# Kernel tuning notes

Measured on AMD Instinct MI355X. Metric: run time of the kernel, lower is better.

## Reference

```python
import jax, jax.numpy as jnp
import numpy as np

N_EMBD = 1024
N_HEAD = 16
HEAD_DIM = N_EMBD // N_HEAD


def setup_inputs() -> dict:
    key = jax.random.key(0)
    ks = jax.random.split(key, 9)
    B, T, C = 4, 2048, N_EMBD
    s = 1.0 / np.sqrt(C)
    return {
        "x": jax.random.normal(ks[0], (B, T, C), jnp.float32),
        "Wq": jax.random.normal(ks[1], (C, C), jnp.float32) * s,
        "bq": jnp.zeros((C,), jnp.float32),
        "Wk": jax.random.normal(ks[2], (C, C), jnp.float32) * s,
        "bk": jnp.zeros((C,), jnp.float32),
        "Wv": jax.random.normal(ks[3], (C, C), jnp.float32) * s,
        "bv": jnp.zeros((C,), jnp.float32),
        "Wp": jax.random.normal(ks[4], (C, C), jnp.float32) * s,
        "bp": jnp.zeros((C,), jnp.float32),
    }


def reference(x, Wq, bq, Wk, bk, Wv, bv, Wp, bp):
    B, T, C = x.shape
    H, D = N_HEAD, HEAD_DIM
    # QKV projections -> (B, H, T, D)
    q = (x @ Wq + bq).reshape(B, T, H, D).transpose(0, 2, 1, 3)
    k = (x @ Wk + bk).reshape(B, T, H, D).transpose(0, 2, 1, 3)
    v = (x @ Wv + bv).reshape(B, T, H, D).transpose(0, 2, 1, 3)
    # scaled scores with causal mask
    att = jnp.einsum("bhtd,bhsd->bhts", q, k) / jnp.sqrt(jnp.asarray(D, x.dtype))
    causal = jnp.tril(jnp.ones((T, T), bool))
    att = jnp.where(causal, att, jnp.asarray(-jnp.inf, att.dtype))
    att = jax.nn.softmax(att, axis=-1)
    # dropout is identity in eval/reference mode
    out = jnp.einsum("bhts,bhsd->bhtd", att, v)
    out = out.transpose(0, 2, 1, 3).reshape(B, T, C)
    return out @ Wp + bp
```

## Files before the change

### kernel.cpp

```cpp
#include <hip/hip_runtime.h>
#include <stdint.h>


typedef __attribute__((ext_vector_type(8))) short bf16x8;
typedef __attribute__((ext_vector_type(8))) ushort u16x8;
typedef __attribute__((ext_vector_type(4))) float f32x4;

__device__ __forceinline__ ushort f2bf(float f) {
  union { float f; uint32_t i; } c; c.f = f;
  uint32_t r = c.i + 0x7fffu + ((c.i >> 16) & 1u);
  return (ushort)(r >> 16);
}
__device__ __forceinline__ uint32_t cvt_pk_bf16(float lo, float hi) {
  uint32_t r;
  asm("v_cvt_pk_bf16_f32 %0, %1, %2" : "=v"(r) : "v"(lo), "v"(hi));
  return r;
}

#define GLOAD16(gp, lp)                                                          \
  __builtin_amdgcn_global_load_lds(                                              \
      (const __attribute__((address_space(1))) unsigned int*)(gp),               \
      (__attribute__((address_space(3))) unsigned int*)(lp), 16, 0, 0)

__global__ __launch_bounds__(256) void f32_to_bf16(const float* __restrict__ in,
                                                   ushort* __restrict__ out, int n) {
  const int i = (blockIdx.x * 256 + threadIdx.x) * 8;
  if (i + 8 > n) return;
  float4 a = *(const float4*)(in + i);
  float4 b = *(const float4*)(in + i + 4);
  u16x8 r;
  r[0] = f2bf(a.x); r[1] = f2bf(a.y); r[2] = f2bf(a.z); r[3] = f2bf(a.w);
  r[4] = f2bf(b.x); r[5] = f2bf(b.y); r[6] = f2bf(b.z); r[7] = f2bf(b.w);
  *(u16x8*)(out + i) = r;
}

__global__ __launch_bounds__(256) void transpose_f32_bf16(const float* __restrict__ W,
                                                          ushort* __restrict__ Wt) {
  __shared__ ushort tile[32][33];
  const int k0 = blockIdx.x * 32, n0 = blockIdx.y * 32;
  const int tx = threadIdx.x & 31, ty = threadIdx.x >> 5;
#pragma unroll
  for (int i = 0; i < 4; ++i)
    tile[ty + i * 8][tx] = f2bf(W[(size_t)(k0 + ty + i * 8) * 1024 + n0 + tx]);
  __syncthreads();
#pragma unroll
  for (int i = 0; i < 4; ++i)
    Wt[(size_t)(n0 + ty + i * 8) * 1024 + k0 + tx] = tile[tx][ty + i * 8];
}

template <int MODE>
__global__ __launch_bounds__(256) void gemm_bt(const ushort* __restrict__ A,
                                               const ushort* __restrict__ Bt,
                                               const float* __restrict__ bias,
                                               void* __restrict__ outp,
                                               int M, int N, int K) {
  __shared__ ushort As[128][32];
  __shared__ ushort Bs[128][32];
  const int tid = threadIdx.x;
  const int lane = tid & 63, wave = tid >> 6;
  const int quad = lane >> 4, l16 = lane & 15;
  const int wy = wave >> 1, wx = wave & 1;
  const int m0 = blockIdx.y * 128, n0 = blockIdx.x * 128;

  const f32x4 fzero = {0.f, 0.f, 0.f, 0.f};
  f32x4 acc[4][4];
#pragma unroll
  for (int i = 0; i < 4; ++i)
#pragma unroll
    for (int j = 0; j < 4; ++j) acc[i][j] = fzero;

  const int r = lane >> 2, ch = (lane & 3) * 8;
  const ushort* Abase = A + (size_t)(m0 + wave * 32 + r) * K + ch;
  const ushort* Bbase = Bt + (size_t)(n0 + wave * 32 + r) * K + ch;

  const int nk = K >> 5;
  for (int kt = 0; kt < nk; ++kt) {
    __syncthreads();
    GLOAD16(Abase + kt * 32,          &As[wave * 32][0]);
    GLOAD16(Abase + 16 * K + kt * 32, &As[wave * 32 + 16][0]);
    GLOAD16(Bbase + kt * 32,          &Bs[wave * 32][0]);
    GLOAD16(Bbase + 16 * K + kt * 32, &Bs[wave * 32 + 16][0]);
    __syncthreads();

    bf16x8 af[4], bfr[4];
#pragma unroll
    for (int i = 0; i < 4; ++i)
      af[i] = *(const bf16x8*)&As[wy * 64 + i * 16 + l16][quad * 8];
#pragma unroll
    for (int j = 0; j < 4; ++j)
      bfr[j] = *(const bf16x8*)&Bs[wx * 64 + j * 16 + l16][quad * 8];
#pragma unroll
    for (int i = 0; i < 4; ++i)
#pragma unroll
      for (int j = 0; j < 4; ++j)
        acc[i][j] = __builtin_amdgcn_mfma_f32_16x16x32_bf16(af[i], bfr[j], acc[i][j], 0, 0, 0);
  }

#pragma unroll
  for (int j = 0; j < 4; ++j) {
    const int col = n0 + wx * 64 + j * 16 + l16;
    const float bv = bias[col];
#pragma unroll
    for (int i = 0; i < 4; ++i) {
#pragma unroll
      for (int rr = 0; rr < 4; ++rr) {
        const int row = m0 + wy * 64 + i * 16 + quad * 4 + rr;
        const float v = acc[i][j][rr] + bv;
        if (MODE == 0) {
          ((float*)outp)[(size_t)row * N + col] = v;
        } else {
          ushort* out = (ushort*)outp;
          const int b = row >> 11, t = row & 2047, h = col >> 6, d = col & 63;
          if (MODE == 1)
            out[(((size_t)(b * 16 + h) * 2048) + t) * 64 + d] = f2bf(v);
          else
            out[(((size_t)(b * 16 + h) * 64) + d) * 2048 + t] = f2bf(v);
        }
      }
    }
  }
}

__global__ __launch_bounds__(256, 3) void attn_kernel(const ushort* __restrict__ q,
                                                      const ushort* __restrict__ k,
                                                      const ushort* __restrict__ v,
                                                      ushort* __restrict__ y) {
  const int T = 2048;
  const int bh = blockIdx.y;
  const int tid = threadIdx.x;
  const int lane = tid & 63, wave = tid >> 6;
  const int quad = lane >> 4, l16 = lane & 15;
  const int rr = lane >> 3, c8 = lane & 7;
  const int swz = l16 & 7;

  __shared__ ushort Qs[128][64];
  __shared__ ushort Ks[64][64];
  __shared__ ushort Vs[64][64];

  const ushort* qp = q + (size_t)bh * T * 64;
  const ushort* kp = k + (size_t)bh * T * 64;
  const ushort* vp = v + (size_t)bh * 64 * T;
  const int b = bh >> 4, h = bh & 15;

  ushort* Pw = &Qs[wave * 32][0];

  const f32x4 fzero = {0.f, 0.f, 0.f, 0.f};
  const float SC = 0.125f * 1.4426950408889634f;

  for (int qsel = 0; qsel < 2; ++qsel) {
    const int qt = qsel ? (15 - (int)blockIdx.x) : (int)blockIdx.x;
    const int qbase = qt * 128;

    __syncthreads();
#pragma unroll
    for (int t = 0; t < 4; ++t) {
      const int row = wave * 32 + t * 8 + rr;
      const int gc = c8 ^ (row & 7);
      GLOAD16(qp + (size_t)(qbase + row) * 64 + gc * 8, &Qs[wave * 32 + t * 8][0]);
    }
    __syncthreads();

    bf16x8 aq[2][2];
#pragma unroll
    for (int i = 0; i < 2; ++i)
#pragma unroll
      for (int kk = 0; kk < 2; ++kk)
        aq[i][kk] = *(const bf16x8*)&Qs[wave * 32 + i * 16 + l16][((4 * kk + quad) ^ swz) * 8];

    f32x4 acc_o[2][4];
    float mstate[2], lstate[2];
#pragma unroll
    for (int i = 0; i < 2; ++i) {
      mstate[i] = -1e30f; lstate[i] = 0.f;
#pragma unroll
      for (int jd = 0; jd < 4; ++jd) acc_o[i][jd] = fzero;
    }

    const int trow0 = qbase + wave * 32;
    const int nkt = qt * 2 + 2;

    for (int kt = 0; kt < nkt; ++kt) {
      __syncthreads();
#pragma unroll
      for (int t = 0; t < 2; ++t) {
        const int row = wave * 16 + t * 8 + rr;
        const int gc = c8 ^ (row & 7);
        GLOAD16(kp + (size_t)(kt * 64 + row) * 64 + gc * 8, &Ks[wave * 16 + t * 8][0]);
        GLOAD16(vp + (size_t)row * T + kt * 64 + gc * 8,    &Vs[wave * 16 + t * 8][0]);
      }
      __syncthreads();

      if (kt * 64 > trow0 + 31) continue;

      bf16x8 ak[4][2];
#pragma unroll
      for (int j = 0; j < 4; ++j)
#pragma unroll
        for (int kk = 0; kk < 2; ++kk)
          ak[j][kk] = *(const bf16x8*)&Ks[j * 16 + l16][((4 * kk + quad) ^ swz) * 8];

#pragma unroll
      for (int i = 0; i < 2; ++i) {
        const int tmin = trow0 + i * 16;
        if (kt * 64 > tmin + 15) continue;
        const int tglob = tmin + l16;

        f32x4 st[4];
#pragma unroll
        for (int j = 0; j < 4; ++j) st[j] = fzero;
#pragma unroll
        for (int j = 0; j < 4; ++j)
#pragma unroll
          for (int kk = 0; kk < 2; ++kk)
            st[j] = __builtin_amdgcn_mfma_f32_16x16x32_bf16(ak[j][kk], aq[i][kk], st[j], 0, 0, 0);

        float mp = -1e30f;
        const bool needmask = (kt * 64 + 63 > tmin);
        if (needmask) {
#pragma unroll
          for (int j = 0; j < 4; ++j)
#pragma unroll
            for (int r2 = 0; r2 < 4; ++r2) {
              const int sg = kt * 64 + j * 16 + quad * 4 + r2;
              float xv = st[j][r2] * SC;
              if (sg > tglob) xv = -1e30f;
              st[j][r2] = xv;
              mp = fmaxf(mp, xv);
            }
        } else {
#pragma unroll
          for (int j = 0; j < 4; ++j)
#pragma unroll
            for (int r2 = 0; r2 < 4; ++r2) {
              const float xv = st[j][r2] * SC;
              st[j][r2] = xv;
              mp = fmaxf(mp, xv);
            }
        }
        mp = fmaxf(mp, __shfl_xor(mp, 16, 64));
        mp = fmaxf(mp, __shfl_xor(mp, 32, 64));

        float mloc = mstate[i];
        const bool defer = (__all(mp - mloc <= 8.0f) != 0);
        if (!defer) {
          const float mnew = fmaxf(mloc, mp);
          const float alpha = exp2f(mloc - mnew);
          mstate[i] = mnew;
          lstate[i] *= alpha;
#pragma unroll
          for (int jd = 0; jd < 4; ++jd) acc_o[i][jd] *= alpha;
          mloc = mnew;
        }
        float rs = 0.f;
#pragma unroll
        for (int j = 0; j < 4; ++j)
#pragma unroll
          for (int r2 = 0; r2 < 4; ++r2) {
            const float p = exp2f(st[j][r2] - mloc);
            st[j][r2] = p;
            rs += p;
          }
        rs += __shfl_xor(rs, 16, 64);
        rs += __shfl_xor(rs, 32, 64);
        lstate[i] += rs;

        ushort* prow = Pw + l16 * 64;
#pragma unroll
        for (int j = 0; j < 4; ++j) {
          uint2 w2;
          w2.x = cvt_pk_bf16(st[j][0], st[j][1]);
          w2.y = cvt_pk_bf16(st[j][2], st[j][3]);
          const int cb = 2 * j + (quad >> 1);
          *(uint2*)(prow + ((cb ^ swz) << 3) + ((quad & 1) << 2)) = w2;
        }
        bf16x8 pb0 = *(const bf16x8*)(prow + ((quad ^ swz) << 3));
        bf16x8 pb1 = *(const bf16x8*)(prow + (((4 + quad) ^ swz) << 3));

#pragma unroll
        for (int jd = 0; jd < 4; ++jd) {
          const int vrow = jd * 16 + l16;
          bf16x8 av0 = *(const bf16x8*)&Vs[vrow][((quad) ^ swz) * 8];
          bf16x8 av1 = *(const bf16x8*)&Vs[vrow][((4 + quad) ^ swz) * 8];
          acc_o[i][jd] = __builtin_amdgcn_mfma_f32_16x16x32_bf16(av0, pb0, acc_o[i][jd], 0, 0, 0);
          acc_o[i][jd] = __builtin_amdgcn_mfma_f32_16x16x32_bf16(av1, pb1, acc_o[i][jd], 0, 0, 0);
        }
      }
    }

#pragma unroll
    for (int i = 0; i < 2; ++i) {
      const int t = trow0 + i * 16 + l16;
      const float inv = 1.0f / lstate[i];
#pragma unroll
      for (int jd = 0; jd < 4; ++jd) {
        uint2 w;
        w.x = cvt_pk_bf16(acc_o[i][jd][0] * inv, acc_o[i][jd][1] * inv);
        w.y = cvt_pk_bf16(acc_o[i][jd][2] * inv, acc_o[i][jd][3] * inv);
        *(uint2*)&y[((size_t)(b * 2048 + t)) * 1024 + h * 64 + jd * 16 + quad * 4] = w;
      }
    }
  }
}

extern "C" void kernel_launch(void* const* d_in, const int* in_sizes, int n_in,
                              void* d_out, int out_size, void* d_ws, size_t ws_size,
                              hipStream_t stream) {
  const float* x  = (const float*)d_in[0];
  const float* Wq = (const float*)d_in[1];
  const float* bq = (const float*)d_in[2];
  const float* Wk = (const float*)d_in[3];
  const float* bk = (const float*)d_in[4];
  const float* Wv = (const float*)d_in[5];
  const float* bv = (const float*)d_in[6];
  const float* Wp = (const float*)d_in[7];
  const float* bp = (const float*)d_in[8];

  ushort* ws  = (ushort*)d_ws;
  ushort* wqt = ws;
  ushort* wkt = wqt + (size_t)1024 * 1024;
  ushort* wvt = wkt + (size_t)1024 * 1024;
  ushort* wpt = wvt + (size_t)1024 * 1024;
  ushort* xb  = wpt + (size_t)1024 * 1024;
  ushort* qq  = xb + (size_t)8192 * 1024;
  ushort* kk  = qq + (size_t)8192 * 1024;
  ushort* vv  = kk + (size_t)8192 * 1024;
  ushort* y   = vv + (size_t)8192 * 1024;

  const dim3 tb(256);
  hipLaunchKernelGGL(f32_to_bf16, dim3(4096), tb, 0, stream, x, xb, 8192 * 1024);
  const dim3 tg(32, 32);
  hipLaunchKernelGGL(transpose_f32_bf16, tg, tb, 0, stream, Wq, wqt);
  hipLaunchKernelGGL(transpose_f32_bf16, tg, tb, 0, stream, Wk, wkt);
  hipLaunchKernelGGL(transpose_f32_bf16, tg, tb, 0, stream, Wv, wvt);
  hipLaunchKernelGGL(transpose_f32_bf16, tg, tb, 0, stream, Wp, wpt);

  const dim3 gg(8, 64);
  hipLaunchKernelGGL((gemm_bt<1>), gg, tb, 0, stream, xb, wqt, bq, (void*)qq, 8192, 1024, 1024);
  hipLaunchKernelGGL((gemm_bt<1>), gg, tb, 0, stream, xb, wkt, bk, (void*)kk, 8192, 1024, 1024);
  hipLaunchKernelGGL((gemm_bt<2>), gg, tb, 0, stream, xb, wvt, bv, (void*)vv, 8192, 1024, 1024);

  const dim3 ag(8, 64);
  hipLaunchKernelGGL(attn_kernel, ag, tb, 0, stream, qq, kk, vv, y);

  hipLaunchKernelGGL((gemm_bt<0>), gg, tb, 0, stream, y, wpt, bp, d_out, 8192, 1024, 1024);
}
```

Baseline: 329.5 us.

## Double-buffer LDS tiles in GEMM and attention, swap grid dimension order

Both the GEMM and the attention kernel now keep two LDS buffers and prefetch the next K/V (or A/B) tile into one while computing on the other. This cuts the per-iteration barrier count from two to one and lets global-to-LDS loads overlap with MFMA work. The grid axes are also swapped so consecutive block IDs walk the M/batch-head dimension, which changes the block scheduling order and cache locality. The cost is double the LDS footprint, which may reduce occupancy in the attention kernel.

```diff
diff --git a/kernel.cpp b/kernel.cpp
--- a/kernel.cpp
+++ b/kernel.cpp
@@ -54,13 +54,13 @@
                                                const float* __restrict__ bias,
                                                void* __restrict__ outp,
                                                int M, int N, int K) {
-  __shared__ ushort As[128][32];
-  __shared__ ushort Bs[128][32];
+  __shared__ ushort As[2][128][32];
+  __shared__ ushort Bs[2][128][32];
   const int tid = threadIdx.x;
   const int lane = tid & 63, wave = tid >> 6;
   const int quad = lane >> 4, l16 = lane & 15;
   const int wy = wave >> 1, wx = wave & 1;
-  const int m0 = blockIdx.y * 128, n0 = blockIdx.x * 128;
+  const int m0 = blockIdx.x * 128, n0 = blockIdx.y * 128;
 
   const f32x4 fzero = {0.f, 0.f, 0.f, 0.f};
   f32x4 acc[4][4];
@@ -73,27 +73,37 @@
   const ushort* Abase = A + (size_t)(m0 + wave * 32 + r) * K + ch;
   const ushort* Bbase = Bt + (size_t)(n0 + wave * 32 + r) * K + ch;
 
+  GLOAD16(Abase,          &As[0][wave * 32][0]);
+  GLOAD16(Abase + 16 * K, &As[0][wave * 32 + 16][0]);
+  GLOAD16(Bbase,          &Bs[0][wave * 32][0]);
+  GLOAD16(Bbase + 16 * K, &Bs[0][wave * 32 + 16][0]);
+  __syncthreads();
+
   const int nk = K >> 5;
+  int cur = 0;
   for (int kt = 0; kt < nk; ++kt) {
-    __syncthreads();
-    GLOAD16(Abase + kt * 32,          &As[wave * 32][0]);
-    GLOAD16(Abase + 16 * K + kt * 32, &As[wave * 32 + 16][0]);
-    GLOAD16(Bbase + kt * 32,          &Bs[wave * 32][0]);
-    GLOAD16(Bbase + 16 * K + kt * 32, &Bs[wave * 32 + 16][0]);
-    __syncthreads();
+    if (kt + 1 < nk) {
+      GLOAD16(Abase + (kt + 1) * 32,          &As[cur ^ 1][wave * 32][0]);
+      GLOAD16(Abase + 16 * K + (kt + 1) * 32, &As[cur ^ 1][wave * 32 + 16][0]);
+      GLOAD16(Bbase + (kt + 1) * 32,          &Bs[cur ^ 1][wave * 32][0]);
+      GLOAD16(Bbase + 16 * K + (kt + 1) * 32, &Bs[cur ^ 1][wave * 32 + 16][0]);
+    }
 
     bf16x8 af[4], bfr[4];
 #pragma unroll
     for (int i = 0; i < 4; ++i)
-      af[i] = *(const bf16x8*)&As[wy * 64 + i * 16 + l16][quad * 8];
+      af[i] = *(const bf16x8*)&As[cur][wy * 64 + i * 16 + l16][quad * 8];
 #pragma unroll
     for (int j = 0; j < 4; ++j)
-      bfr[j] = *(const bf16x8*)&Bs[wx * 64 + j * 16 + l16][quad * 8];
+      bfr[j] = *(const bf16x8*)&Bs[cur][wx * 64 + j * 16 + l16][quad * 8];
 #pragma unroll
     for (int i = 0; i < 4; ++i)
 #pragma unroll
       for (int j = 0; j < 4; ++j)
         acc[i][j] = __builtin_amdgcn_mfma_f32_16x16x32_bf16(af[i], bfr[j], acc[i][j], 0, 0, 0);
+
+    __syncthreads();
+    cur ^= 1;
   }
 
 #pragma unroll
@@ -126,7 +136,7 @@
                                                       const ushort* __restrict__ v,
                                                       ushort* __restrict__ y) {
   const int T = 2048;
-  const int bh = blockIdx.y;
+  const int bh = blockIdx.x;
   const int tid = threadIdx.x;
   const int lane = tid & 63, wave = tid >> 6;
   const int quad = lane >> 4, l16 = lane & 15;
@@ -134,8 +144,8 @@
   const int swz = l16 & 7;
 
   __shared__ ushort Qs[128][64];
-  __shared__ ushort Ks[64][64];
-  __shared__ ushort Vs[64][64];
+  __shared__ ushort Ks[2][64][64];
+  __shared__ ushort Vs[2][64][64];
 
   const ushort* qp = q + (size_t)bh * T * 64;
   const ushort* kp = k + (size_t)bh * T * 64;
@@ -148,7 +158,7 @@
   const float SC = 0.125f * 1.4426950408889634f;
 
   for (int qsel = 0; qsel < 2; ++qsel) {
-    const int qt = qsel ? (15 - (int)blockIdx.x) : (int)blockIdx.x;
+    const int qt = qsel ? (15 - (int)blockIdx.y) : (int)blockIdx.y;
     const int qbase = qt * 128;
 
     __syncthreads();
@@ -179,112 +189,127 @@
     const int trow0 = qbase + wave * 32;
     const int nkt = qt * 2 + 2;
 
+#pragma unroll
+    for (int t = 0; t < 2; ++t) {
+      const int row = wave * 16 + t * 8 + rr;
+      const int gc = c8 ^ (row & 7);
+      GLOAD16(kp + (size_t)row * 64 + gc * 8,          &Ks[0][wave * 16 + t * 8][0]);
+      GLOAD16(vp + (size_t)row * T + gc * 8,           &Vs[0][wave * 16 + t * 8][0]);
+    }
+    __syncthreads();
+
+    int cur = 0;
     for (int kt = 0; kt < nkt; ++kt) {
-      __syncthreads();
-#pragma unroll
-      for (int t = 0; t < 2; ++t) {
-        const int row = wave * 16 + t * 8 + rr;
-        const int gc = c8 ^ (row & 7);
-        GLOAD16(kp + (size_t)(kt * 64 + row) * 64 + gc * 8, &Ks[wave * 16 + t * 8][0]);
-        GLOAD16(vp + (size_t)row * T + kt * 64 + gc * 8,    &Vs[wave * 16 + t * 8][0]);
-      }
-      __syncthreads();
-
-      if (kt * 64 > trow0 + 31) continue;
-
-      bf16x8 ak[4][2];
-#pragma unroll
-      for (int j = 0; j < 4; ++j)
-#pragma unroll
-        for (int kk = 0; kk < 2; ++kk)
-          ak[j][kk] = *(const bf16x8*)&Ks[j * 16 + l16][((4 * kk + quad) ^ swz) * 8];
-
-#pragma unroll
-      for (int i = 0; i < 2; ++i) {
-        const int tmin = trow0 + i * 16;
-        if (kt * 64 > tmin + 15) continue;
-        const int tglob = tmin + l16;
-
-        f32x4 st[4];
-#pragma unroll
-        for (int j = 0; j < 4; ++j) st[j] = fzero;
-#pragma unroll
-        for (int j = 0; j < 4; ++j)
-#pragma unroll
-          for (int kk = 0; kk < 2; ++kk)
-            st[j] = __builtin_amdgcn_mfma_f32_16x16x32_bf16(ak[j][kk], aq[i][kk], st[j], 0, 0, 0);
-
-        float mp = -1e30f;
-        const bool needmask = (kt * 64 + 63 > tmin);
-        if (needmask) {
-#pragma unroll
-          for (int j = 0; j < 4; ++j)
-#pragma unroll
-            for (int r2 = 0; r2 < 4; ++r2) {
-              const int sg = kt * 64 + j * 16 + quad * 4 + r2;
-              float xv = st[j][r2] * SC;
-              if (sg > tglob) xv = -1e30f;
-              st[j][r2] = xv;
-              mp = fmaxf(mp, xv);
-            }
-        } else {
-#pragma unroll
-          for (int j = 0; j < 4; ++j)
-#pragma unroll
-            for (int r2 = 0; r2 < 4; ++r2) {
-              const float xv = st[j][r2] * SC;
-              st[j][r2] = xv;
-              mp = fmaxf(mp, xv);
-            }
-        }
-        mp = fmaxf(mp, __shfl_xor(mp, 16, 64));
-        mp = fmaxf(mp, __shfl_xor(mp, 32, 64));
-
-        float mloc = mstate[i];
-        const bool defer = (__all(mp - mloc <= 8.0f) != 0);
-        if (!defer) {
-          const float mnew = fmaxf(mloc, mp);
-          const float alpha = exp2f(mloc - mnew);
-          mstate[i] = mnew;
-          lstate[i] *= alpha;
-#pragma unroll
-          for (int jd = 0; jd < 4; ++jd) acc_o[i][jd] *= alpha;
-          mloc = mnew;
-        }
-        float rs = 0.f;
-#pragma unroll
-        for (int j = 0; j < 4; ++j)
-#pragma unroll
-          for (int r2 = 0; r2 < 4; ++r2) {
-            const float p = exp2f(st[j][r2] - mloc);
-            st[j][r2] = p;
-            rs += p;
-          }
-        rs += __shfl_xor(rs, 16, 64);
-        rs += __shfl_xor(rs, 32, 64);
-        lstate[i] += rs;
-
-        ushort* prow = Pw + l16 * 64;
-#pragma unroll
-        for (int j = 0; j < 4; ++j) {
-          uint2 w2;
-          w2.x = cvt_pk_bf16(st[j][0], st[j][1]);
-          w2.y = cvt_pk_bf16(st[j][2], st[j][3]);
-          const int cb = 2 * j + (quad >> 1);
-          *(uint2*)(prow + ((cb ^ swz) << 3) + ((quad & 1) << 2)) = w2;
-        }
-        bf16x8 pb0 = *(const bf16x8*)(prow + ((quad ^ swz) << 3));
-        bf16x8 pb1 = *(const bf16x8*)(prow + (((4 + quad) ^ swz) << 3));
-
-#pragma unroll
-        for (int jd = 0; jd < 4; ++jd) {
-          const int vrow = jd * 16 + l16;
-          bf16x8 av0 = *(const bf16x8*)&Vs[vrow][((quad) ^ swz) * 8];
-          bf16x8 av1 = *(const bf16x8*)&Vs[vrow][((4 + quad) ^ swz) * 8];
-          acc_o[i][jd] = __builtin_amdgcn_mfma_f32_16x16x32_bf16(av0, pb0, acc_o[i][jd], 0, 0, 0);
-          acc_o[i][jd] = __builtin_amdgcn_mfma_f32_16x16x32_bf16(av1, pb1, acc_o[i][jd], 0, 0, 0);
+      if (kt + 1 < nkt) {
+#pragma unroll
+        for (int t = 0; t < 2; ++t) {
+          const int row = wave * 16 + t * 8 + rr;
+          const int gc = c8 ^ (row & 7);
+          GLOAD16(kp + (size_t)((kt + 1) * 64 + row) * 64 + gc * 8,
+                  &Ks[cur ^ 1][wave * 16 + t * 8][0]);
+          GLOAD16(vp + (size_t)row * T + (kt + 1) * 64 + gc * 8,
+                  &Vs[cur ^ 1][wave * 16 + t * 8][0]);
         }
       }
+
+      if (!(kt * 64 > trow0 + 31)) {
+        bf16x8 ak[4][2];
+#pragma unroll
+        for (int j = 0; j < 4; ++j)
+#pragma unroll
+          for (int kk = 0; kk < 2; ++kk)
+            ak[j][kk] = *(const bf16x8*)&Ks[cur][j * 16 + l16][((4 * kk + quad) ^ swz) * 8];
+
+#pragma unroll
+        for (int i = 0; i < 2; ++i) {
+          const int tmin = trow0 + i * 16;
+          if (kt * 64 > tmin + 15) continue;
+          const int tglob = tmin + l16;
+
+          f32x4 st[4];
+#pragma unroll
+          for (int j = 0; j < 4; ++j) st[j] = fzero;
+#pragma unroll
+          for (int j = 0; j < 4; ++j)
+#pragma unroll
+            for (int kk = 0; kk < 2; ++kk)
+              st[j] = __builtin_amdgcn_mfma_f32_16x16x32_bf16(ak[j][kk], aq[i][kk], st[j], 0, 0, 0);
+
+          float mp = -1e30f;
+          const bool needmask = (kt * 64 + 63 > tmin);
+          if (needmask) {
+#pragma unroll
+            for (int j = 0; j < 4; ++j)
+#pragma unroll
+              for (int r2 = 0; r2 < 4; ++r2) {
+                const int sg = kt * 64 + j * 16 + quad * 4 + r2;
+                float xv = st[j][r2] * SC;
+                if (sg > tglob) xv = -1e30f;
+                st[j][r2] = xv;
+                mp = fmaxf(mp, xv);
+              }
+          } else {
+#pragma unroll
+            for (int j = 0; j < 4; ++j)
+#pragma unroll
+              for (int r2 = 0; r2 < 4; ++r2) {
+                const float xv = st[j][r2] * SC;
+                st[j][r2] = xv;
+                mp = fmaxf(mp, xv);
+              }
+          }
+          mp = fmaxf(mp, __shfl_xor(mp, 16, 64));
+          mp = fmaxf(mp, __shfl_xor(mp, 32, 64));
+
+          float mloc = mstate[i];
+          const bool defer = (__all(mp - mloc <= 8.0f) != 0);
+          if (!defer) {
+            const float mnew = fmaxf(mloc, mp);
+            const float alpha = exp2f(mloc - mnew);
+            mstate[i] = mnew;
+            lstate[i] *= alpha;
+#pragma unroll
+            for (int jd = 0; jd < 4; ++jd) acc_o[i][jd] *= alpha;
+            mloc = mnew;
+          }
+          float rs = 0.f;
+#pragma unroll
+          for (int j = 0; j < 4; ++j)
+#pragma unroll
+            for (int r2 = 0; r2 < 4; ++r2) {
+              const float p = exp2f(st[j][r2] - mloc);
+              st[j][r2] = p;
+              rs += p;
+            }
+          rs += __shfl_xor(rs, 16, 64);
+          rs += __shfl_xor(rs, 32, 64);
+          lstate[i] += rs;
+
+          ushort* prow = Pw + l16 * 64;
+#pragma unroll
+          for (int j = 0; j < 4; ++j) {
+            uint2 w2;
+            w2.x = cvt_pk_bf16(st[j][0], st[j][1]);
+            w2.y = cvt_pk_bf16(st[j][2], st[j][3]);
+            const int cb = 2 * j + (quad >> 1);
+            *(uint2*)(prow + ((cb ^ swz) << 3) + ((quad & 1) << 2)) = w2;
+          }
+          bf16x8 pb0 = *(const bf16x8*)(prow + ((quad ^ swz) << 3));
+          bf16x8 pb1 = *(const bf16x8*)(prow + (((4 + quad) ^ swz) << 3));
+
+#pragma unroll
+          for (int jd = 0; jd < 4; ++jd) {
+            const int vrow = jd * 16 + l16;
+            bf16x8 av0 = *(const bf16x8*)&Vs[cur][vrow][((quad) ^ swz) * 8];
+            bf16x8 av1 = *(const bf16x8*)&Vs[cur][vrow][((4 + quad) ^ swz) * 8];
+            acc_o[i][jd] = __builtin_amdgcn_mfma_f32_16x16x32_bf16(av0, pb0, acc_o[i][jd], 0, 0, 0);
+            acc_o[i][jd] = __builtin_amdgcn_mfma_f32_16x16x32_bf16(av1, pb1, acc_o[i][jd], 0, 0, 0);
+          }
+        }
+      }
+
+      __syncthreads();
+      cur ^= 1;
     }
 
 #pragma unroll
@@ -334,12 +359,12 @@
   hipLaunchKernelGGL(transpose_f32_bf16, tg, tb, 0, stream, Wv, wvt);
   hipLaunchKernelGGL(transpose_f32_bf16, tg, tb, 0, stream, Wp, wpt);
 
-  const dim3 gg(8, 64);
+  const dim3 gg(64, 8);
   hipLaunchKernelGGL((gemm_bt<1>), gg, tb, 0, stream, xb, wqt, bq, (void*)qq, 8192, 1024, 1024);
   hipLaunchKernelGGL((gemm_bt<1>), gg, tb, 0, stream, xb, wkt, bk, (void*)kk, 8192, 1024, 1024);
   hipLaunchKernelGGL((gemm_bt<2>), gg, tb, 0, stream, xb, wvt, bv, (void*)vv, 8192, 1024, 1024);
 
-  const dim3 ag(8, 64);
+  const dim3 ag(64, 8);
   hipLaunchKernelGGL(attn_kernel, ag, tb, 0, stream, qq, kk, vv, y);
 
   hipLaunchKernelGGL((gemm_bt<0>), gg, tb, 0, stream, y, wpt, bp, d_out, 8192, 1024, 1024);
```

Result: faster. 309.8 us (-6.0%).
